# Optimization experiments

Hardware: AMD Instinct MI355X
Metric: run time of the kernel (lower is better)

Reference implementation:

```python
import jax, jax.numpy as jnp
import numpy as np

N_BINS = 15


def setup_inputs() -> dict:
    key = jax.random.key(0)
    k1, k2 = jax.random.split(key)
    N, C = 2097152, 100
    logits = jax.random.normal(k1, (N, C), dtype=jnp.float32)
    labels = jax.random.randint(k2, (N,), 0, C, dtype=jnp.int32)
    return {"logits": logits, "labels": labels}


def reference(logits, labels):
    # probs -> per-sample confidence (max prob) and prediction (argmax)
    probs = jax.nn.softmax(logits, axis=-1)          # [N, C]
    conf = jnp.max(probs, axis=-1)                   # [N]
    pred = jnp.argmax(probs, axis=-1)                # [N]
    acc = (pred == labels).astype(conf.dtype)        # [N]

    # Torch loop uses half-open bins (lower, upper]; searchsorted 'left' on the
    # boundaries returns first i with b[i] >= conf, so bin = i - 1. conf == 0
    # would fall in no bin (gt(0) fails) -> bin_idx = -1 -> masked out.
    boundaries = jnp.linspace(0.0, 1.0, N_BINS + 1).astype(conf.dtype)
    bin_idx = jnp.searchsorted(boundaries, conf, side="left") - 1  # [N]
    w = (bin_idx >= 0).astype(conf.dtype)
    seg = jnp.clip(bin_idx, 0, N_BINS - 1)

    # Single fused histogram pass: counts, confidence sums, correct sums per bin.
    counts = jax.ops.segment_sum(w, seg, num_segments=N_BINS)
    conf_sum = jax.ops.segment_sum(conf * w, seg, num_segments=N_BINS)
    acc_sum = jax.ops.segment_sum(acc * w, seg, num_segments=N_BINS)

    n = jnp.asarray(conf.shape[0], conf.dtype)
    prop = counts / n
    denom = jnp.maximum(counts, 1.0)
    avg_conf = conf_sum / denom
    avg_acc = acc_sum / denom
    ece = jnp.sum(jnp.where(counts > 0, jnp.abs(avg_conf - avg_acc) * prop, 0.0))
    return ece.reshape(1)
```

## Files before the change

kernel.cpp:

```cpp
#include <hip/hip_runtime.h>

#define NBINS 15
#define NCLS  100

__global__ void ece_init_kernel(float* __restrict__ gbins) {
    int i = threadIdx.x;
    if (i < 3 * NBINS) gbins[i] = 0.0f;
}

__global__ __launch_bounds__(256) void ece_main_kernel(
        const float* __restrict__ logits,
        const int*   __restrict__ labels,
        float*       __restrict__ gbins,
        int n_rows)
{
    __shared__ float sb[3 * NBINS];
    for (int i = threadIdx.x; i < 3 * NBINS; i += blockDim.x) sb[i] = 0.0f;
    __syncthreads();

    const int stride = gridDim.x * blockDim.x;
    for (int r = blockIdx.x * blockDim.x + threadIdx.x; r < n_rows; r += stride) {
        const float4* row = reinterpret_cast<const float4*>(logits + (size_t)r * NCLS);

        float m  = -3.402823466e+38f;
        int   ix = 0;
        float s0 = 0.0f, s1 = 0.0f, s2 = 0.0f, s3 = 0.0f;

        #pragma unroll
        for (int i = 0; i < NCLS / 4; ++i) {
            float4 v = row[i];
            s0 += __expf(v.x);
            s1 += __expf(v.y);
            s2 += __expf(v.z);
            s3 += __expf(v.w);
            bool g;
            g = v.x > m; ix = g ? 4 * i + 0 : ix; m = g ? v.x : m;
            g = v.y > m; ix = g ? 4 * i + 1 : ix; m = g ? v.y : m;
            g = v.z > m; ix = g ? 4 * i + 2 : ix; m = g ? v.z : m;
            g = v.w > m; ix = g ? 4 * i + 3 : ix; m = g ? v.w : m;
        }

        float s    = (s0 + s1) + (s2 + s3);
        float conf = __expf(m) / s;
        float acc  = (ix == labels[r]) ? 1.0f : 0.0f;

        int bin = 0;
        #pragma unroll
        for (int i = 1; i <= NBINS; ++i)
            bin += (conf > (float)i * (1.0f / 15.0f)) ? 1 : 0;
        bin = min(bin, NBINS - 1);

        atomicAdd(&sb[bin],             1.0f);
        atomicAdd(&sb[NBINS + bin],     conf);
        atomicAdd(&sb[2 * NBINS + bin], acc);
    }

    __syncthreads();
    if (threadIdx.x < 3 * NBINS) atomicAdd(&gbins[threadIdx.x], sb[threadIdx.x]);
}

__global__ void ece_final_kernel(const float* __restrict__ gbins,
                                 float* __restrict__ out,
                                 float inv_n)
{
    int lane = threadIdx.x;
    float term = 0.0f;
    if (lane < NBINS) {
        float cnt = gbins[lane];
        if (cnt > 0.0f) {
            float cs = gbins[NBINS + lane];
            float as = gbins[2 * NBINS + lane];
            term = fabsf(cs - as) * inv_n;
        }
    }
    #pragma unroll
    for (int off = 32; off >= 1; off >>= 1)
        term += __shfl_down(term, off);
    if (lane == 0) out[0] = term;
}

extern "C" void kernel_launch(void* const* d_in, const int* in_sizes, int n_in,
                              void* d_out, int out_size, void* d_ws, size_t ws_size,
                              hipStream_t stream) {
    const float* logits = (const float*)d_in[0];
    const int*   labels = (const int*)d_in[1];
    const int    n_rows = in_sizes[1];

    float* gbins = (float*)d_ws;
    float* out   = (float*)d_out;

    ece_init_kernel<<<1, 64, 0, stream>>>(gbins);

    ece_main_kernel<<<1024, 256, 0, stream>>>(logits, labels, gbins, n_rows);

    ece_final_kernel<<<1, 64, 0, stream>>>(gbins, out, 1.0f / (float)n_rows);
}
```

Measured before the change: 1.068 ms.

## Stage logits tiles into LDS with coalesced global_load_lds before per-row reduction

Replaces per-thread strided row loads from global memory with a coalesced cooperative copy of a 128-row tile into LDS using direct global-to-LDS loads. Each thread then reduces its row from shared memory. Block size and grid size change, and a tail path handles leftover rows. Uncoalesced global accesses should drop, at the cost of large LDS use per block, lower occupancy, possible bank conflicts, and no overlap between loading and compute.

Result: faster. 1.045 ms (-2.1%).

```diff
diff --git a/kernel.cpp b/kernel.cpp
--- a/kernel.cpp
+++ b/kernel.cpp
@@ -2,61 +2,98 @@
 
 #define NBINS 15
 #define NCLS  100
+#define TROWS 128
+#define NF4   (NCLS / 4)
+#define GRID  768
 
 __global__ void ece_init_kernel(float* __restrict__ gbins) {
     int i = threadIdx.x;
     if (i < 3 * NBINS) gbins[i] = 0.0f;
 }
 
-__global__ __launch_bounds__(256) void ece_main_kernel(
+__device__ __forceinline__ void row_stats(const float4* __restrict__ row,
+                                          float& conf, int& ix)
+{
+    float m  = -3.402823466e+38f;
+    float s0 = 0.0f, s1 = 0.0f, s2 = 0.0f, s3 = 0.0f;
+    ix = 0;
+    #pragma unroll
+    for (int i = 0; i < NF4; ++i) {
+        float4 v = row[i];
+        s0 += __expf(v.x);
+        s1 += __expf(v.y);
+        s2 += __expf(v.z);
+        s3 += __expf(v.w);
+        bool g;
+        g = v.x > m; ix = g ? 4 * i + 0 : ix; m = g ? v.x : m;
+        g = v.y > m; ix = g ? 4 * i + 1 : ix; m = g ? v.y : m;
+        g = v.z > m; ix = g ? 4 * i + 2 : ix; m = g ? v.z : m;
+        g = v.w > m; ix = g ? 4 * i + 3 : ix; m = g ? v.w : m;
+    }
+    conf = __expf(m) / ((s0 + s1) + (s2 + s3));
+}
+
+__device__ __forceinline__ int bin_of(float conf) {
+    int bin = 0;
+    #pragma unroll
+    for (int i = 1; i <= NBINS; ++i)
+        bin += (conf > (float)i * (1.0f / 15.0f)) ? 1 : 0;
+    return min(bin, NBINS - 1);
+}
+
+__global__ __launch_bounds__(TROWS) void ece_main_kernel(
         const float* __restrict__ logits,
         const int*   __restrict__ labels,
         float*       __restrict__ gbins,
         int n_rows)
 {
+    __shared__ float tile[TROWS * NCLS];
     __shared__ float sb[3 * NBINS];
-    for (int i = threadIdx.x; i < 3 * NBINS; i += blockDim.x) sb[i] = 0.0f;
-    __syncthreads();
 
-    const int stride = gridDim.x * blockDim.x;
-    for (int r = blockIdx.x * blockDim.x + threadIdx.x; r < n_rows; r += stride) {
-        const float4* row = reinterpret_cast<const float4*>(logits + (size_t)r * NCLS);
+    const int t = threadIdx.x;
+    for (int i = t; i < 3 * NBINS; i += TROWS) sb[i] = 0.0f;
 
-        float m  = -3.402823466e+38f;
-        int   ix = 0;
-        float s0 = 0.0f, s1 = 0.0f, s2 = 0.0f, s3 = 0.0f;
+    const int n_tiles = n_rows / TROWS;
+    for (int tl = blockIdx.x; tl < n_tiles; tl += gridDim.x) {
+        __syncthreads();
 
+        const float* gsrc = logits + (size_t)tl * (TROWS * NCLS);
         #pragma unroll
-        for (int i = 0; i < NCLS / 4; ++i) {
-            float4 v = row[i];
-            s0 += __expf(v.x);
-            s1 += __expf(v.y);
-            s2 += __expf(v.z);
-            s3 += __expf(v.w);
-            bool g;
-            g = v.x > m; ix = g ? 4 * i + 0 : ix; m = g ? v.x : m;
-            g = v.y > m; ix = g ? 4 * i + 1 : ix; m = g ? v.y : m;
-            g = v.z > m; ix = g ? 4 * i + 2 : ix; m = g ? v.z : m;
-            g = v.w > m; ix = g ? 4 * i + 3 : ix; m = g ? v.w : m;
+        for (int k = 0; k < NF4; ++k) {
+            const int idx = (k * TROWS + t) * 4;
+            __builtin_amdgcn_global_load_lds(
+                (const __attribute__((address_space(1))) unsigned int*)(gsrc + idx),
+                (__attribute__((address_space(3)))       unsigned int*)(tile + idx),
+                16, 0, 0);
         }
+        const int lbl = labels[(size_t)tl * TROWS + t];
 
-        float s    = (s0 + s1) + (s2 + s3);
-        float conf = __expf(m) / s;
-        float acc  = (ix == labels[r]) ? 1.0f : 0.0f;
+        __syncthreads();
 
-        int bin = 0;
-        #pragma unroll
-        for (int i = 1; i <= NBINS; ++i)
-            bin += (conf > (float)i * (1.0f / 15.0f)) ? 1 : 0;
-        bin = min(bin, NBINS - 1);
-
+        float conf; int ix;
+        row_stats(reinterpret_cast<const float4*>(tile + t * NCLS), conf, ix);
+        const float acc = (ix == lbl) ? 1.0f : 0.0f;
+        const int   bin = bin_of(conf);
         atomicAdd(&sb[bin],             1.0f);
         atomicAdd(&sb[NBINS + bin],     conf);
         atomicAdd(&sb[2 * NBINS + bin], acc);
     }
 
+    if (blockIdx.x == 0) {
+        for (int r = n_tiles * TROWS + t; r < n_rows; r += TROWS) {
+            float conf; int ix;
+            row_stats(reinterpret_cast<const float4*>(logits + (size_t)r * NCLS),
+                      conf, ix);
+            const float acc = (ix == labels[r]) ? 1.0f : 0.0f;
+            const int   bin = bin_of(conf);
+            atomicAdd(&sb[bin],             1.0f);
+            atomicAdd(&sb[NBINS + bin],     conf);
+            atomicAdd(&sb[2 * NBINS + bin], acc);
+        }
+    }
+
     __syncthreads();
-    if (threadIdx.x < 3 * NBINS) atomicAdd(&gbins[threadIdx.x], sb[threadIdx.x]);
+    if (t < 3 * NBINS) atomicAdd(&gbins[t], sb[t]);
 }
 
 __global__ void ece_final_kernel(const float* __restrict__ gbins,
@@ -91,7 +128,7 @@
 
     ece_init_kernel<<<1, 64, 0, stream>>>(gbins);
 
-    ece_main_kernel<<<1024, 256, 0, stream>>>(logits, labels, gbins, n_rows);
+    ece_main_kernel<<<GRID, TROWS, 0, stream>>>(logits, labels, gbins, n_rows);
 
     ece_final_kernel<<<1, 64, 0, stream>>>(gbins, out, 1.0f / (float)n_rows);
 }
```
